# Kernel optimization log

Measured on AMD Instinct MI355X. Metric: run time of the kernel, lower is better.

The kernel has to match this reference:

```python
import jax, jax.numpy as jnp
import numpy as np

B, T, E, H, D_PRICE = 16, 2048, 128, 4, 512


def setup_inputs() -> dict:
    key = jax.random.key(0)
    ks = jax.random.split(key, 22)
    f32 = jnp.float32

    def w(k, shape):
        fan_in = shape[0]
        return (jax.random.normal(k, shape, f32) / np.sqrt(fan_in)).astype(f32)

    def b(k, n):
        return (jax.random.normal(k, (n,), f32) * 0.01).astype(f32)

    inp = {
        # OHLC prices, positive, normalized scale
        "ohlc": jax.random.uniform(ks[0], (B, T, 4), f32, 0.5, 1.5),
        # ohlc_proj: Linear(4, 64)
        "Wp": w(ks[1], (4, 64)), "bp": b(ks[2], 64),
        # curvature_net: Linear(64,128) -> ReLU -> Linear(128,32)
        "Wc1": w(ks[3], (64, 128)), "bc1": b(ks[4], 128),
        "Wc2": w(ks[5], (128, 32)), "bc2": b(ks[6], 32),
        # volatility_net: Linear(64,64) -> ReLU -> Linear(64,16)
        "Wv1": w(ks[7], (64, 64)), "bv1": b(ks[8], 64),
        "Wv2": w(ks[9], (64, 16)), "bv2": b(ks[10], 16),
        # sr_field_net: Linear(64,64) -> ReLU -> Linear(64,16)
        "Ws1": w(ks[11], (64, 64)), "bs1": b(ks[12], 64),
        "Ws2": w(ks[13], (64, 16)), "bs2": b(ks[14], 16),
        # MultiheadAttention(embed_dim=128, num_heads=4): fused in-proj + out-proj
        "Wqkv": w(ks[15], (E, 3 * E)), "bqkv": b(ks[16], 3 * E),
        "Wo": w(ks[17], (E, E)), "bo": b(ks[18], E),
        # output_proj: Linear(128, d_price)
        "Wout": w(ks[19], (E, D_PRICE)), "bout": b(ks[20], D_PRICE),
    }
    return inp


def _mlp(x, W1, b1, W2, b2):
    return jax.nn.relu(x @ W1 + b1) @ W2 + b2


def reference(ohlc, Wp, bp, Wc1, bc1, Wc2, bc2, Wv1, bv1, Wv2, bv2,
              Ws1, bs1, Ws2, bs2, Wqkv, bqkv, Wo, bo, Wout, bout):
    # NB: compute_curvature / compute_volatility_surface / detect_sr_levels
    # in the original forward are dead code (results never used), so they are
    # omitted here; output math is identical.
    e = ohlc @ Wp + bp                                   # [B,T,64]
    feats = jnp.concatenate([
        e,
        _mlp(e, Wc1, bc1, Wc2, bc2),                     # [B,T,32]
        _mlp(e, Wv1, bv1, Wv2, bv2),                     # [B,T,16]
        _mlp(e, Ws1, bs1, Ws2, bs2),                     # [B,T,16]
    ], axis=-1)                                          # [B,T,128]

    Bn, Tn, En = feats.shape
    dh = En // H
    qkv = feats @ Wqkv + bqkv                            # [B,T,3E]
    q, k, v = jnp.split(qkv, 3, axis=-1)

    def heads(x):
        return x.reshape(Bn, Tn, H, dh).transpose(0, 2, 1, 3)  # [B,H,T,dh]

    q, k, v = heads(q), heads(k), heads(v)
    scores = jnp.einsum('bhqd,bhkd->bhqk', q, k) / np.sqrt(dh).astype(feats.dtype)
    a = jax.nn.softmax(scores, axis=-1)                  # [B,H,T,T]
    o = jnp.einsum('bhqk,bhkd->bhqd', a, v)
    o = o.transpose(0, 2, 1, 3).reshape(Bn, Tn, En)
    attended = o @ Wo + bo                               # [B,T,128]

    pooled = attended.mean(axis=1)                       # [B,128]
    return pooled @ Wout + bout                          # [B,512]
```

## Files before the change

### kernel.cpp

```cpp
#include <hip/hip_runtime.h>


typedef __attribute__((ext_vector_type(4)))  float f32x4;
typedef __attribute__((ext_vector_type(4)))  short short4v;
typedef __attribute__((ext_vector_type(8)))  short short8v;

static __device__ __forceinline__ unsigned short f2b(float f) {
    unsigned int u = __builtin_bit_cast(unsigned int, f);
    u += 0x7fffu + ((u >> 16) & 1u);
    return (unsigned short)(u >> 16);
}

static __device__ __forceinline__ unsigned int cvtpk_bf16(float a, float b) {
    unsigned int r;
    asm volatile("v_cvt_pk_bf16_f32 %0, %1, %2" : "=v"(r) : "v"(a), "v"(b));
    return r;
}

__global__ __launch_bounds__(256) void prep_kernel(
    const float* Wqkv, const float* Wc1, const float* Wc2, const float* Wv1,
    const float* Wv2, const float* Ws1, const float* Ws2,
    unsigned short* wqkvt, unsigned short* wc1t, unsigned short* wc2t,
    unsigned short* wv1t, unsigned short* wv2t, unsigned short* ws1t,
    unsigned short* ws2t, float* pooled, float* qkmax)
{
    int tid = threadIdx.x;
    if (blockIdx.x < 48) {
        __shared__ float tile[32][33];
        int bidn = blockIdx.x % 12, bidk = blockIdx.x / 12;
        int n0 = bidn * 32, k0 = bidk * 32;
        {
            int r = tid >> 3, cq = tid & 7;
            float4 v = *(const float4*)(Wqkv + (size_t)(k0 + r) * 384 + n0 + cq * 4);
            tile[r][cq*4+0] = v.x; tile[r][cq*4+1] = v.y;
            tile[r][cq*4+2] = v.z; tile[r][cq*4+3] = v.w;
        }
        __syncthreads();
        {
            int nr = tid >> 3, kq = tid & 7;
            union { unsigned short us[4]; short4v v; } pk;
#pragma unroll
            for (int j = 0; j < 4; ++j) pk.us[j] = f2b(tile[kq*4+j][nr]);
            *(short4v*)(wqkvt + (size_t)(n0 + nr) * 128 + k0 + kq * 4) = pk.v;
        }
        return;
    }
    int idx = (blockIdx.x - 48) * 256 + tid;
    if (idx < 8192)  { int n = idx >> 6, kk = idx & 63;  wc1t[idx] = f2b(Wc1[kk*128 + n]); return; }
    idx -= 8192;
    if (idx < 4096)  { int n = idx >> 7, kk = idx & 127; wc2t[idx] = f2b(Wc2[kk*32  + n]); return; }
    idx -= 4096;
    if (idx < 4096)  { int n = idx >> 6, kk = idx & 63;  wv1t[idx] = f2b(Wv1[kk*64  + n]); return; }
    idx -= 4096;
    if (idx < 1024)  { int n = idx >> 6, kk = idx & 63;  wv2t[idx] = f2b(Wv2[kk*16  + n]); return; }
    idx -= 1024;
    if (idx < 4096)  { int n = idx >> 6, kk = idx & 63;  ws1t[idx] = f2b(Ws1[kk*64  + n]); return; }
    idx -= 4096;
    if (idx < 1024)  { int n = idx >> 6, kk = idx & 63;  ws2t[idx] = f2b(Ws2[kk*16  + n]); return; }
    idx -= 1024;
    if (idx < 2048)  { pooled[idx] = 0.f; return; }
    idx -= 2048;
    if (idx < 128)   qkmax[idx] = 0.f;
}

template<int N, int K>
static __device__ __forceinline__ void stage_w(
    const unsigned short* __restrict__ wt, char* Bs, int tid)
{
    constexpr int SL = K / 8;
#pragma unroll
    for (int c = tid; c < N * SL; c += 256) {
        int n = c / SL, s = c % SL;
        short8v v = *(const short8v*)(wt + n * K + s * 8);
        *(short8v*)(Bs + n * (K * 2) + ((s ^ (n & (SL - 1))) << 4)) = v;
    }
}

template<int N, int K, int A_ROWB, int D_ROWB, bool RELU, bool TO_LDS>
static __device__ __forceinline__ void tile_gemm_l(
    const char* As, const char* Bs, const float* __restrict__ bias, char* dst,
    unsigned short* __restrict__ gOut, int ocol, int m0, int w, int lane)
{
    constexpr int ASL = A_ROWB / 16, DSL = D_ROWB / 16, BSL = K / 8;
    constexpr int NT = N / 16, KS = K / 32;
    int l15 = lane & 15, hi4 = lane >> 4;
    f32x4 acc[NT];
#pragma unroll
    for (int nt = 0; nt < NT; ++nt)
#pragma unroll
        for (int r = 0; r < 4; ++r) acc[nt][r] = 0.f;

#pragma unroll
    for (int ks = 0; ks < KS; ++ks) {
        int slot = ks * 4 + hi4;
        int m = w * 16 + l15;
        short8v af = *(const short8v*)(As + m * A_ROWB + ((slot ^ (m & (ASL - 1))) << 4));
#pragma unroll
        for (int nt = 0; nt < NT; ++nt) {
            int n = nt * 16 + l15;
            short8v bf = *(const short8v*)(Bs + n * (K * 2) + ((slot ^ (n & (BSL - 1))) << 4));
            acc[nt] = __builtin_amdgcn_mfma_f32_16x16x32_bf16(af, bf, acc[nt], 0, 0, 0);
        }
    }
#pragma unroll
    for (int nt = 0; nt < NT; ++nt) {
        int n = nt * 16 + l15;
        float bv = bias[n];
#pragma unroll
        for (int r = 0; r < 4; ++r) {
            int m = w * 16 + hi4 * 4 + r;
            float v = acc[nt][r] + bv;
            if (RELU) v = fmaxf(v, 0.f);
            if (TO_LDS) {
                *(unsigned short*)(dst + m * D_ROWB + (((n >> 3) ^ (m & (DSL - 1))) << 4) + (n & 7) * 2) = f2b(v);
            } else {
                gOut[(size_t)(m0 + m) * 128 + ocol + n] = f2b(v);
            }
        }
    }
}

__global__ __launch_bounds__(256) void fused_mlp(
    const float* __restrict__ ohlc, const float* __restrict__ Wp, const float* __restrict__ bp,
    const unsigned short* __restrict__ wc1t, const float* __restrict__ bc1,
    const unsigned short* __restrict__ wc2t, const float* __restrict__ bc2,
    const unsigned short* __restrict__ wv1t, const float* __restrict__ bv1,
    const unsigned short* __restrict__ wv2t, const float* __restrict__ bv2,
    const unsigned short* __restrict__ ws1t, const float* __restrict__ bs1,
    const unsigned short* __restrict__ ws2t, const float* __restrict__ bs2,
    unsigned short* __restrict__ feats)
{
    __shared__ float wp[256];
    __shared__ float bpl[64];
    __shared__ char Et[64 * 128];
    __shared__ char Ht[64 * 256];
    __shared__ char Bw1[16384];
    __shared__ char Bw2[8192];

    int tid = threadIdx.x;
    int m0 = blockIdx.x * 64;
    int branch = blockIdx.y;
    wp[tid] = Wp[tid];
    if (tid < 64) bpl[tid] = bp[tid];

    if (branch == 0)      { stage_w<128, 64>(wc1t, Bw1, tid); stage_w<32, 128>(wc2t, Bw2, tid); }
    else if (branch == 1) { stage_w< 64, 64>(wv1t, Bw1, tid); stage_w<16,  64>(wv2t, Bw2, tid); }
    else                  { stage_w< 64, 64>(ws1t, Bw1, tid); stage_w<16,  64>(ws2t, Bw2, tid); }
    __syncthreads();

    {
        int tok = tid >> 2, jq = tid & 3;
        float4 ov = ((const float4*)ohlc)[m0 + tok];
#pragma unroll
        for (int c = 0; c < 2; ++c) {
            int sl = jq * 2 + c;
            union { unsigned short us[8]; short8v v; } pk;
#pragma unroll
            for (int jj = 0; jj < 8; ++jj) {
                int j = sl * 8 + jj;
                float e = bpl[j] + ov.x * wp[j] + ov.y * wp[64 + j]
                                 + ov.z * wp[128 + j] + ov.w * wp[192 + j];
                pk.us[jj] = f2b(e);
            }
            *(short8v*)(Et + tok * 128 + ((sl ^ (tok & 7)) << 4)) = pk.v;
            if (branch == 0)
                *(short8v*)(feats + (size_t)(m0 + tok) * 128 + sl * 8) = pk.v;
        }
    }

    int lane = tid & 63, w = tid >> 6;
    if (branch == 0) {
        tile_gemm_l<128, 64, 128, 256, true, true >(Et, Bw1, bc1, Ht, feats, 0,  m0, w, lane);
        tile_gemm_l< 32, 128, 256, 256, false, false>(Ht, Bw2, bc2, Ht, feats, 64, m0, w, lane);
    } else if (branch == 1) {
        tile_gemm_l< 64, 64, 128, 128, true, true >(Et, Bw1, bv1, Ht, feats, 0,  m0, w, lane);
        tile_gemm_l< 16, 64, 128, 128, false, false>(Ht, Bw2, bv2, Ht, feats, 96, m0, w, lane);
    } else {
        tile_gemm_l< 64, 64, 128, 128, true, true >(Et, Bw1, bs1, Ht, feats, 0,   m0, w, lane);
        tile_gemm_l< 16, 64, 128, 128, false, false>(Ht, Bw2, bs2, Ht, feats, 112, m0, w, lane);
    }
}

__global__ __launch_bounds__(256) void qkv_gemm(
    const unsigned short* __restrict__ feats,
    const unsigned short* __restrict__ wqkvt, const float* __restrict__ bqkv,
    unsigned short* __restrict__ qg, unsigned short* __restrict__ kg,
    unsigned short* __restrict__ vt2, float* __restrict__ qkmax)
{
    constexpr int ROWB = 256, CPR = 16;
    __shared__ short8v smemv[4096];
    char* As = (char*)smemv;
    char* Bs = (char*)smemv + 32768;

    int tid = threadIdx.x;
    int m0 = blockIdx.x * 128;
    int sel = blockIdx.y;
    const unsigned short* BT = wqkvt + (size_t)sel * 128 * 128;

    for (int c = tid; c < 128 * CPR; c += 256) {
        int m = c / CPR, s = c % CPR;
        short8v v = *(const short8v*)(feats + (size_t)(m0 + m) * 128 + s * 8);
        *(short8v*)(As + m * ROWB + ((s ^ (m & 15)) * 16)) = v;
    }
    for (int c = tid; c < 128 * CPR; c += 256) {
        int n = c / CPR, s = c % CPR;
        short8v v = *(const short8v*)(BT + (size_t)n * 128 + s * 8);
        *(short8v*)(Bs + n * ROWB + ((s ^ (n & 15)) * 16)) = v;
    }
    __syncthreads();

    int lane = tid & 63, w = tid >> 6;
    int l15 = lane & 15, hi4 = lane >> 4;

    f32x4 acc[2][8];
#pragma unroll
    for (int mt = 0; mt < 2; ++mt)
#pragma unroll
        for (int nt = 0; nt < 8; ++nt)
#pragma unroll
            for (int r = 0; r < 4; ++r) acc[mt][nt][r] = 0.f;

#pragma unroll
    for (int ks = 0; ks < 4; ++ks) {
        int slot = ks * 4 + hi4;
        short8v af[2];
#pragma unroll
        for (int mt = 0; mt < 2; ++mt) {
            int m = w * 32 + mt * 16 + l15;
            af[mt] = *(const short8v*)(As + m * ROWB + ((slot ^ (m & 15)) * 16));
        }
#pragma unroll
        for (int nt = 0; nt < 8; ++nt) {
            int n = nt * 16 + l15;
            short8v bf = *(const short8v*)(Bs + n * ROWB + ((slot ^ (n & 15)) * 16));
            acc[0][nt] = __builtin_amdgcn_mfma_f32_16x16x32_bf16(af[0], bf, acc[0][nt], 0, 0, 0);
            acc[1][nt] = __builtin_amdgcn_mfma_f32_16x16x32_bf16(af[1], bf, acc[1][nt], 0, 0, 0);
        }
    }

    const float QSCALE = 1.4426950408889634f * 0.17677669529663687f;
    int b = m0 >> 11, tp0 = m0 & 2047;

    if (sel == 2) {
#pragma unroll
        for (int mt = 0; mt < 2; ++mt)
#pragma unroll
            for (int nt = 0; nt < 8; ++nt) {
                int n = nt * 16 + l15;
                float bv = bqkv[256 + n];
                int h = n >> 5, dh = n & 31;
                uint2 pk;
                pk.x = cvtpk_bf16(acc[mt][nt][0] + bv, acc[mt][nt][1] + bv);
                pk.y = cvtpk_bf16(acc[mt][nt][2] + bv, acc[mt][nt][3] + bv);
                int g32 = (tp0 >> 5) + w;
                size_t o = (size_t)(b * 4 + h) * 65536 + (size_t)g32 * 1024
                         + dh * 32 + hi4 * 8 + mt * 4;
                *(uint2*)(vt2 + o) = pk;
            }
    } else {
        float amax[4] = {0.f, 0.f, 0.f, 0.f};
        float scale = (sel == 0) ? QSCALE : 1.0f;
#pragma unroll
        for (int mt = 0; mt < 2; ++mt)
#pragma unroll
            for (int nt = 0; nt < 8; ++nt) {
                int n = nt * 16 + l15;
                float bv = bqkv[sel * 128 + n];
#pragma unroll
                for (int r = 0; r < 4; ++r) {
                    float v = (acc[mt][nt][r] + bv) * scale;
                    amax[nt >> 1] = fmaxf(amax[nt >> 1], fabsf(v));
                    int m = w * 32 + mt * 16 + hi4 * 4 + r;
                    *(unsigned short*)(As + m * 256 + (((n >> 3) ^ (m & 7)) << 4) + (n & 7) * 2) = f2b(v);
                }
            }
#pragma unroll
        for (int g = 0; g < 4; ++g) {
            float mv = amax[g];
            mv = fmaxf(mv, __shfl_xor(mv, 1));  mv = fmaxf(mv, __shfl_xor(mv, 2));
            mv = fmaxf(mv, __shfl_xor(mv, 4));  mv = fmaxf(mv, __shfl_xor(mv, 8));
            mv = fmaxf(mv, __shfl_xor(mv, 16)); mv = fmaxf(mv, __shfl_xor(mv, 32));
            if (lane == 0)
                atomicMax((int*)(qkmax + sel * 64 + b * 4 + g), __float_as_int(mv));
        }
        __syncthreads();
        unsigned short* og = (sel == 0) ? qg : kg;
#pragma unroll
        for (int it = 0; it < 8; ++it) {
            int ch = it * 256 + tid;
            int m = ch >> 4, c = ch & 15;
            short8v vv = *(const short8v*)(As + m * 256 + ((c ^ (m & 7)) << 4));
            int h = c >> 2, dq = c & 3;
            *(short8v*)(og + ((size_t)(b * 4 + h) * 2048 + tp0 + m) * 32 + dq * 8) = vv;
        }
    }
}

__global__ __launch_bounds__(256) void attn_kernel(
    const unsigned short* __restrict__ qg, const unsigned short* __restrict__ kg,
    const unsigned short* __restrict__ vt2, const float* __restrict__ qkmax,
    float* __restrict__ pooled)
{
    __shared__ char Kv[2][4096];

    int tid = threadIdx.x, bid = blockIdx.x;
    int bh = bid & 63, qc = bid >> 6;
    int b = bh >> 2;
    int lane = tid & 63, w = tid >> 6;
    int l15 = lane & 15, h = (lane >> 4) & 3;
    int q0 = qc * 128 + w * 32;

    const char* qp = (const char*)qg + ((size_t)bh * 2048 + q0) * 64 + l15 * 64 + h * 16;
    short8v Qf[2];
    Qf[0] = *(const short8v*)(qp);
    Qf[1] = *(const short8v*)(qp + 1024);

    float negM0 = -(32.0f * qkmax[bh] * qkmax[64 + bh]);
    f32x4 NEGM4 = {negM0, negM0, negM0, negM0};

    f32x4 accO[2][2], lacc[2];
#pragma unroll
    for (int j = 0; j < 2; ++j)
#pragma unroll
        for (int r = 0; r < 4; ++r) { accO[j][0][r] = 0.f; accO[j][1][r] = 0.f; lacc[j][r] = 0.f; }

    short8v ONES;
    {
        union { unsigned short us[8]; short8v v; } u;
#pragma unroll
        for (int j = 0; j < 8; ++j) u.us[j] = 0x3F80;
        ONES = u.v;
    }

    const char* gk = (const char*)kg  + (size_t)bh * 131072;
    const char* gv = (const char*)vt2 + (size_t)bh * 131072;
    const char* gsrc = (tid < 128) ? (gk + tid * 16) : (gv + (tid - 128) * 16);
    int ldst = tid * 16;
    int foff = l15 * 64 + h * 16;

    auto compute = [&](const char* bufp) {
        short8v Ka = *(const short8v*)(bufp + foff);
        short8v Kb = *(const short8v*)(bufp + 1024 + foff);
        short8v Va = *(const short8v*)(bufp + 2048 + foff);
        short8v Vb = *(const short8v*)(bufp + 3072 + foff);
        __builtin_amdgcn_s_setprio(1);
        union { unsigned int u[4]; short8v v; } pk[2];
#pragma unroll
        for (int tau = 0; tau < 2; ++tau) {
            short8v Kf = tau ? Kb : Ka;
#pragma unroll
            for (int j = 0; j < 2; ++j) {
                f32x4 s = __builtin_amdgcn_mfma_f32_16x16x32_bf16(Kf, Qf[j], NEGM4, 0, 0, 0);
                float p0 = __builtin_amdgcn_exp2f(s[0]);
                float p1 = __builtin_amdgcn_exp2f(s[1]);
                float p2 = __builtin_amdgcn_exp2f(s[2]);
                float p3 = __builtin_amdgcn_exp2f(s[3]);
                pk[j].u[tau * 2 + 0] = cvtpk_bf16(p0, p1);
                pk[j].u[tau * 2 + 1] = cvtpk_bf16(p2, p3);
            }
        }
#pragma unroll
        for (int j = 0; j < 2; ++j) {
            lacc[j]    = __builtin_amdgcn_mfma_f32_16x16x32_bf16(ONES, pk[j].v, lacc[j], 0, 0, 0);
            accO[j][0] = __builtin_amdgcn_mfma_f32_16x16x32_bf16(Va,   pk[j].v, accO[j][0], 0, 0, 0);
            accO[j][1] = __builtin_amdgcn_mfma_f32_16x16x32_bf16(Vb,   pk[j].v, accO[j][1], 0, 0, 0);
        }
        __builtin_amdgcn_s_setprio(0);
    };

    short8v R;
    R = *(const short8v*)(gsrc);
    *(short8v*)(Kv[0] + ldst) = R;
    R = *(const short8v*)(gsrc + 2048);
    __syncthreads();

    const char* gp = gsrc + 2 * 2048;
#pragma unroll 1
    for (int g = 0; g < 62; g += 2) {
        *(short8v*)(Kv[1] + ldst) = R;
        short8v R2 = *(const short8v*)(gp);
        compute(Kv[0]);
        __syncthreads();
        *(short8v*)(Kv[0] + ldst) = R2;
        R = *(const short8v*)(gp + 2048);
        gp += 4096;
        compute(Kv[1]);
        __syncthreads();
    }
    *(short8v*)(Kv[1] + ldst) = R;
    compute(Kv[0]);
    __syncthreads();
    compute(Kv[1]);

    float o8[2][4];
#pragma unroll
    for (int d = 0; d < 2; ++d)
#pragma unroll
        for (int r = 0; r < 4; ++r) o8[d][r] = 0.f;
#pragma unroll
    for (int j = 0; j < 2; ++j) {
        float inv = 1.0f / (lacc[j][0] + 1e-30f);
#pragma unroll
        for (int d = 0; d < 2; ++d)
#pragma unroll
            for (int r = 0; r < 4; ++r) o8[d][r] += accO[j][d][r] * inv;
    }
#pragma unroll
    for (int d = 0; d < 2; ++d)
#pragma unroll
        for (int r = 0; r < 4; ++r) {
            float v = o8[d][r];
            v += __shfl_xor(v, 1); v += __shfl_xor(v, 2);
            v += __shfl_xor(v, 4); v += __shfl_xor(v, 8);
            if (l15 == 0) {
                int dh = d * 16 + h * 4 + r;
                atomicAdd(pooled + b * 128 + (bh & 3) * 32 + dh, v);
            }
        }
}

__global__ __launch_bounds__(256) void head_kernel(
    const float* __restrict__ pooled, const float* __restrict__ Wo,
    const float* __restrict__ bo, const float* __restrict__ Wout,
    const float* __restrict__ bout, float* __restrict__ out)
{
    int bq = blockIdx.x, tid = threadIdx.x;
    __shared__ float pl[128], mid[128];
    if (tid < 128) pl[tid] = pooled[bq * 128 + tid] * (1.f / 2048.f);
    __syncthreads();
    if (tid < 128) {
        float s = bo[tid];
#pragma unroll 4
        for (int c = 0; c < 128; ++c) s += pl[c] * Wo[c * 128 + tid];
        mid[tid] = s;
    }
    __syncthreads();
    for (int j = tid; j < 512; j += 256) {
        float s = bout[j];
#pragma unroll 4
        for (int i = 0; i < 128; ++i) s += mid[i] * Wout[i * 512 + j];
        out[bq * 512 + j] = s;
    }
}

extern "C" void kernel_launch(void* const* d_in, const int* in_sizes, int n_in,
                              void* d_out, int out_size, void* d_ws, size_t ws_size,
                              hipStream_t stream) {
    (void)in_sizes; (void)n_in; (void)out_size; (void)ws_size;
    const float* ohlc = (const float*)d_in[0];
    const float* Wp   = (const float*)d_in[1];  const float* bp   = (const float*)d_in[2];
    const float* Wc1  = (const float*)d_in[3];  const float* bc1  = (const float*)d_in[4];
    const float* Wc2  = (const float*)d_in[5];  const float* bc2  = (const float*)d_in[6];
    const float* Wv1  = (const float*)d_in[7];  const float* bv1  = (const float*)d_in[8];
    const float* Wv2  = (const float*)d_in[9];  const float* bv2  = (const float*)d_in[10];
    const float* Ws1  = (const float*)d_in[11]; const float* bs1  = (const float*)d_in[12];
    const float* Ws2  = (const float*)d_in[13]; const float* bs2  = (const float*)d_in[14];
    const float* Wqkv = (const float*)d_in[15]; const float* bqkv = (const float*)d_in[16];
    const float* Wo   = (const float*)d_in[17]; const float* bo   = (const float*)d_in[18];
    const float* Wout = (const float*)d_in[19]; const float* bout = (const float*)d_in[20];
    float* out = (float*)d_out;
    char* ws = (char*)d_ws;

    const size_t MB8 = 8388608;
    unsigned short* feats = (unsigned short*)(ws);
    unsigned short* qg    = (unsigned short*)(ws + 1 * MB8);
    unsigned short* kg    = (unsigned short*)(ws + 2 * MB8);
    unsigned short* vt2   = (unsigned short*)(ws + 3 * MB8);
    float*          pooled = (float*)(ws + 4 * MB8);
    float*          qkmax  = (float*)(ws + 4 * MB8 + 8192);
    unsigned short* wc1t  = (unsigned short*)(ws + 4 * MB8 + 8192 + 512);
    unsigned short* wc2t  = wc1t + 8192;
    unsigned short* wv1t  = wc2t + 4096;
    unsigned short* wv2t  = wv1t + 4096;
    unsigned short* ws1t  = wv2t + 1024;
    unsigned short* ws2t  = ws1t + 4096;
    unsigned short* wqkvt = ws2t + 1024;

    prep_kernel<<<145, 256, 0, stream>>>(Wqkv, Wc1, Wc2, Wv1, Wv2, Ws1, Ws2,
                                         wqkvt, wc1t, wc2t, wv1t, wv2t, ws1t, ws2t,
                                         pooled, qkmax);
    fused_mlp<<<dim3(512, 3), 256, 0, stream>>>(ohlc, Wp, bp, wc1t, bc1, wc2t, bc2,
                                                wv1t, bv1, wv2t, bv2, ws1t, bs1, ws2t, bs2, feats);
    qkv_gemm<<<dim3(256, 3), 256, 0, stream>>>(feats, wqkvt, bqkv, qg, kg, vt2, qkmax);
    attn_kernel<<<1024, 256, 0, stream>>>(qg, kg, vt2, qkmax, pooled);
    head_kernel<<<16, 256, 0, stream>>>(pooled, Wo, bo, Wout, bout, out);
}
```

Baseline: 130.5 us.

## Load K/V fragments directly from global into registers, drop LDS staging

The attention kernel no longer stages K and V tiles through a double-buffered shared-memory buffer with block barriers. Each lane now loads its own MFMA fragments straight from global memory into registers, double-buffered with a one-tile prefetch. This removes the LDS writes, the LDS reads and the __syncthreads, and drops the s_setprio hints. In exchange, each of the four waves loads the same K/V data independently, so the kernel issues four times as many global and L2 loads and uses more registers.

```diff
diff --git a/kernel.cpp b/kernel.cpp
--- a/kernel.cpp
+++ b/kernel.cpp
@@ -301,8 +301,6 @@
     const unsigned short* __restrict__ vt2, const float* __restrict__ qkmax,
     float* __restrict__ pooled)
 {
-    __shared__ char Kv[2][4096];
-
     int tid = threadIdx.x, bid = blockIdx.x;
     int bh = bid & 63, qc = bid >> 6;
     int b = bh >> 2;
@@ -332,18 +330,10 @@
         ONES = u.v;
     }
 
-    const char* gk = (const char*)kg  + (size_t)bh * 131072;
-    const char* gv = (const char*)vt2 + (size_t)bh * 131072;
-    const char* gsrc = (tid < 128) ? (gk + tid * 16) : (gv + (tid - 128) * 16);
-    int ldst = tid * 16;
-    int foff = l15 * 64 + h * 16;
-
-    auto compute = [&](const char* bufp) {
-        short8v Ka = *(const short8v*)(bufp + foff);
-        short8v Kb = *(const short8v*)(bufp + 1024 + foff);
-        short8v Va = *(const short8v*)(bufp + 2048 + foff);
-        short8v Vb = *(const short8v*)(bufp + 3072 + foff);
-        __builtin_amdgcn_s_setprio(1);
+    const char* kc = (const char*)kg  + (size_t)bh * 131072 + l15 * 64 + h * 16;
+    const char* vc = (const char*)vt2 + (size_t)bh * 131072 + l15 * 64 + h * 16;
+
+    auto compute = [&](short8v Ka, short8v Kb, short8v Va, short8v Vb) {
         union { unsigned int u[4]; short8v v; } pk[2];
 #pragma unroll
         for (int tau = 0; tau < 2; ++tau) {
@@ -365,32 +355,35 @@
             accO[j][0] = __builtin_amdgcn_mfma_f32_16x16x32_bf16(Va,   pk[j].v, accO[j][0], 0, 0, 0);
             accO[j][1] = __builtin_amdgcn_mfma_f32_16x16x32_bf16(Vb,   pk[j].v, accO[j][1], 0, 0, 0);
         }
-        __builtin_amdgcn_s_setprio(0);
     };
 
-    short8v R;
-    R = *(const short8v*)(gsrc);
-    *(short8v*)(Kv[0] + ldst) = R;
-    R = *(const short8v*)(gsrc + 2048);
-    __syncthreads();
-
-    const char* gp = gsrc + 2 * 2048;
+    short8v KaE, KbE, VaE, VbE, KaO, KbO, VaO, VbO;
+    KaE = *(const short8v*)(kc);
+    KbE = *(const short8v*)(kc + 1024);
+    VaE = *(const short8v*)(vc);
+    VbE = *(const short8v*)(vc + 1024);
+
 #pragma unroll 1
-    for (int g = 0; g < 62; g += 2) {
-        *(short8v*)(Kv[1] + ldst) = R;
-        short8v R2 = *(const short8v*)(gp);
-        compute(Kv[0]);
-        __syncthreads();
-        *(short8v*)(Kv[0] + ldst) = R2;
-        R = *(const short8v*)(gp + 2048);
-        gp += 4096;
-        compute(Kv[1]);
-        __syncthreads();
-    }
-    *(short8v*)(Kv[1] + ldst) = R;
-    compute(Kv[0]);
-    __syncthreads();
-    compute(Kv[1]);
+    for (int g = 0; g < 64; g += 2) {
+        {
+            const char* kn = kc + (size_t)(g + 1) * 2048;
+            const char* vn = vc + (size_t)(g + 1) * 2048;
+            KaO = *(const short8v*)(kn);
+            KbO = *(const short8v*)(kn + 1024);
+            VaO = *(const short8v*)(vn);
+            VbO = *(const short8v*)(vn + 1024);
+        }
+        compute(KaE, KbE, VaE, VbE);
+        if (g + 2 < 64) {
+            const char* kn = kc + (size_t)(g + 2) * 2048;
+            const char* vn = vc + (size_t)(g + 2) * 2048;
+            KaE = *(const short8v*)(kn);
+            KbE = *(const short8v*)(kn + 1024);
+            VaE = *(const short8v*)(vn);
+            VbE = *(const short8v*)(vn + 1024);
+        }
+        compute(KaO, KbO, VaO, VbO);
+    }
 
     float o8[2][4];
 #pragma unroll
```

Result: slower. 143.6 us (+10.0%).
